# Optimization experiments

Measured on AMD Instinct MI355X. Metric: run time of the kernel, lower is better.

Reference implementation:

```python
import jax, jax.numpy as jnp
import numpy as np

B, S, E, H = 4, 2048, 1024, 16
D = E // H


def setup_inputs() -> dict:
    key = jax.random.key(0)
    ks = jax.random.split(key, 6)
    scale = 1.0 / np.sqrt(E).astype(np.float32)
    return {
        "x": jax.random.normal(ks[0], (B, S, E), jnp.float32),
        # positive entries -> cumsum normalizer is well conditioned
        "weight": jax.random.uniform(ks[1], (H, S), jnp.float32, 0.05, 1.0),
        "bias": jax.random.normal(ks[2], (H, S), jnp.float32) * 0.02,
        "inp_w": jax.random.normal(ks[3], (E, E), jnp.float32) * scale,
        "inp_b": jax.random.normal(ks[4], (E,), jnp.float32) * 0.02,
        "out_w": jax.random.normal(ks[5], (E, E), jnp.float32) * scale,
    }


def reference(x, weight, bias, inp_w, inp_b, out_w):
    Bx, Sx, Ex = x.shape
    Hx = weight.shape[0]
    Dx = Ex // Hx
    # input projection (torch Linear: x @ W.T + b)
    x = x @ inp_w.T + inp_b
    # (B,S,E) -> (B,E,S) -> (B,H,D,S)
    xh = x.transpose(0, 2, 1).reshape(Bx, Hx, Dx, Sx)
    # Toeplitz causal matrix per head: M[h,i,j] = weight[h, j-i] if j>=i else 0
    idx = jnp.arange(Sx)
    off = idx[None, :] - idx[:, None]  # (S,S)
    M = jnp.where(off >= 0, weight[:, off], jnp.zeros((), x.dtype))  # (H,S,S)
    # batched matmul over the sequence axis: y[b,h,d,t] = sum_s x[b,h,d,s] M[h,s,t]
    y = jnp.einsum('bhds,hst->bhdt', xh, M)
    # cumulative-sum normalization (do_toep_mean=True)
    norm = jnp.cumsum(weight, axis=-1)  # (H,S)
    y = y / norm[None, :, None, :]
    # per-head, per-position bias
    y = y + bias[None, :, None, :]
    # (B,H,D,S) -> (B,E,S) -> (B,S,E)
    y = y.reshape(Bx, Ex, Sx).transpose(0, 2, 1)
    # output projection (no bias)
    return y @ out_w.T
```

## Files before the change

kernel.cpp:

```cpp
#include <hip/hip_runtime.h>

typedef unsigned short u16;
typedef __attribute__((ext_vector_type(4))) float f32x4;
typedef __attribute__((ext_vector_type(8))) short short8;
typedef __attribute__((ext_vector_type(8))) __bf16 bf16x8;

__device__ __forceinline__ u16 f2bf(float f) {
  unsigned u = __builtin_bit_cast(unsigned, f);
  u = u + 0x7fffu + ((u >> 16) & 1u);
  return (u16)(u >> 16);
}

__device__ __forceinline__ void load_lds16(const void* g, void* l) {
  __builtin_amdgcn_global_load_lds((__attribute__((address_space(1))) void*)g,
                                   (__attribute__((address_space(3))) void*)l,
                                   16, 0, 0);
}

__global__ __launch_bounds__(256) void prep_all(const float* __restrict__ x,
                                                const float* __restrict__ inp_w,
                                                const float* __restrict__ out_w,
                                                const float* __restrict__ weight,
                                                u16* __restrict__ Xb,
                                                u16* __restrict__ Wb,
                                                u16* __restrict__ OWb,
                                                float* __restrict__ normB,
                                                u16* __restrict__ V) {
  const int bx = blockIdx.x, tid = threadIdx.x;
  if (bx < 10240) {
    const float* src; u16* dst; int i;
    if (bx < 8192)      { src = x;     dst = Xb;  i = bx * 256 + tid; }
    else if (bx < 9216) { src = inp_w; dst = Wb;  i = (bx - 8192) * 256 + tid; }
    else                { src = out_w; dst = OWb; i = (bx - 9216) * 256 + tid; }
    const float4 v = ((const float4*)src)[i];
    ushort4 o;
    o.x = f2bf(v.x); o.y = f2bf(v.y); o.z = f2bf(v.z); o.w = f2bf(v.w);
    ((ushort4*)dst)[i] = o;
    return;
  }
  if (bx < 10256) {
    const int h = bx - 10240;
    __shared__ float ts[256];
    float v[8];
    const float* src = weight + h * 2048 + tid * 8;
    float s = 0.f;
#pragma unroll
    for (int j = 0; j < 8; ++j) v[j] = src[j];
#pragma unroll
    for (int j = 0; j < 8; ++j) { s += v[j]; v[j] = s; }
    ts[tid] = s;
    __syncthreads();
    float xx = s;
#pragma unroll
    for (int d = 1; d < 256; d <<= 1) {
      float y = (tid >= d) ? ts[tid - d] : 0.f;
      __syncthreads();
      xx += y;
      ts[tid] = xx;
      __syncthreads();
    }
    const float excl = xx - s;
    float* dst = normB + h * 2048 + tid * 8;
#pragma unroll
    for (int j = 0; j < 8; ++j) dst[j] = excl + v[j];
    return;
  }
  {
    const int bb = bx - 10256;
    const int h = bb & 15, tb = bb >> 4;
    __shared__ u16 wl[2048];
#pragma unroll
    for (int j = 0; j < 8; ++j) wl[tid * 8 + j] = f2bf(weight[h * 2048 + tid * 8 + j]);
    __syncthreads();
#pragma unroll
    for (int i = 0; i < 8; ++i) {
      const int cid = i * 256 + tid;
      const int row = cid >> 4, c = cid & 15;
      const int t = tb * 128 + row;
      const int j0 = c * 8;
      unsigned v[8];
#pragma unroll
      for (int jj = 0; jj < 8; ++jj) {
        const int j = j0 + jj;
        v[jj] = (t >= j) ? (unsigned)wl[t - j] : 0u;
      }
      uint4 o;
      o.x = v[0] | (v[1] << 16); o.y = v[2] | (v[3] << 16);
      o.z = v[4] | (v[5] << 16); o.w = v[6] | (v[7] << 16);
      *(uint4*)(V + ((size_t)(h * 2048 + t)) * 128 + j0) = o;
    }
  }
}

template <bool BIAS, bool F32OUT, int GX>
__global__ __launch_bounds__(256) void gemm_nt4(const u16* __restrict__ A,
                                                const u16* __restrict__ B,
                                                void* __restrict__ C,
                                                const float* __restrict__ bias,
                                                int K, int lda, int ldb, int ldc) {
  __shared__ __align__(16) u16 As[2][128 * 64];
  __shared__ __align__(16) u16 Bs[2][128 * 64];
  const int tid = threadIdx.x;
  const int lane = tid & 63, wv = tid >> 6;
  const int wm = wv >> 1, wn = wv & 1;
  const int l15 = lane & 15, g = lane >> 4;

  const int flat = (int)blockIdx.x;
  const int sw = (flat & 7) * 64 + (flat >> 3);
  const int m0 = (sw / GX) * 128, n0 = (sw % GX) * 128;

  const int NT = K >> 6;

  auto stage = [&](int t, int bi) {
    const int kt = t << 6;
#pragma unroll
    for (int i = 0; i < 4; ++i) {
      const int c = i * 256 + tid;
      const int row = c >> 3, cc = c & 7;
      load_lds16(A + (size_t)(m0 + row) * lda + kt + ((cc ^ (row & 7)) << 3),
                 &As[bi][i * 2048 + wv * 512]);
    }
#pragma unroll
    for (int i = 0; i < 4; ++i) {
      const int c = i * 256 + tid;
      const int row = c >> 3, cc = c & 7;
      load_lds16(B + (size_t)(n0 + row) * ldb + kt + ((cc ^ (row & 7)) << 3),
                 &Bs[bi][i * 2048 + wv * 512]);
    }
  };

  f32x4 acc[4][4] = {};
  stage(0, 0);
  __syncthreads();
  int cur = 0;
  for (int t = 0; t < NT; ++t) {
    if (t + 1 < NT) stage(t + 1, cur ^ 1);
#pragma unroll
    for (int kh = 0; kh < 2; ++kh) {
      bf16x8 af[4], bf[4];
#pragma unroll
      for (int mf = 0; mf < 4; ++mf) {
        const int row = wm * 64 + mf * 16 + l15;
        af[mf] = *(const bf16x8*)(&As[cur][row * 64 + ((((kh << 2) + g) ^ (row & 7)) << 3)]);
      }
#pragma unroll
      for (int nf = 0; nf < 4; ++nf) {
        const int row = wn * 64 + nf * 16 + l15;
        bf[nf] = *(const bf16x8*)(&Bs[cur][row * 64 + ((((kh << 2) + g) ^ (row & 7)) << 3)]);
      }
      __builtin_amdgcn_s_setprio(1);
#pragma unroll
      for (int mf = 0; mf < 4; ++mf)
#pragma unroll
        for (int nf = 0; nf < 4; ++nf)
          acc[mf][nf] = __builtin_amdgcn_mfma_f32_16x16x32_bf16(af[mf], bf[nf],
                                                                acc[mf][nf], 0, 0, 0);
      __builtin_amdgcn_s_setprio(0);
    }
    __syncthreads();
    cur ^= 1;
  }

#pragma unroll
  for (int mf = 0; mf < 4; ++mf) {
#pragma unroll
    for (int r = 0; r < 4; ++r) {
      const int row = m0 + wm * 64 + mf * 16 + g * 4 + r;
      const float bb = BIAS ? bias[row] : 0.f;
#pragma unroll
      for (int nf = 0; nf < 4; ++nf) {
        const int col = n0 + wn * 64 + nf * 16 + l15;
        const float v = acc[mf][nf][r] + bb;
        if (F32OUT)
          ((float*)C)[(size_t)row * ldc + col] = v;
        else
          ((u16*)C)[(size_t)row * ldc + col] = f2bf(v);
      }
    }
  }
}

__global__ __launch_bounds__(256) void toep_conv(const u16* __restrict__ X1t,
                                                 const u16* __restrict__ V,
                                                 const float* __restrict__ normB,
                                                 const float* __restrict__ biasB,
                                                 u16* __restrict__ Y2b) {
  __shared__ __align__(16) u16 As[3][128 * 64];
  __shared__ __align__(16) u16 Xs[3][64 * 64];
  const int tid = threadIdx.x;
  const int lane = tid & 63, wv = tid >> 6;
  const int l15 = lane & 15, g = lane >> 4;

  const int x = (int)blockIdx.x;
  const int h = (x & 7) + 8 * ((x >> 3) & 1);
  const int pb = x >> 4;
  const int pair = pb & 7, b = pb >> 3;

  const u16* Vh = V + (size_t)h * 2048 * 128;
  const u16* Xrow = X1t + (size_t)h * 64 * 8192 + b * 2048;

#pragma unroll 1
  for (int ti = 0; ti < 2; ++ti) {
    const int tt = ti ? pair : 15 - pair;
    const int t0 = tt * 128;
    const int Q = (tt + 1) * 2;
    f32x4 acc[2][4] = {};

    auto stage = [&](int q, int bufi) {
      const int st = q >> 1, k = q & 1;
      const u16* Ab = Vh + (size_t)(tt - st) * 128 * 128 + k * 64;
#pragma unroll
      for (int i = 0; i < 4; ++i) {
        const int c = i * 256 + tid;
        const int row = c >> 3, cc = c & 7;
        load_lds16(Ab + row * 128 + ((cc ^ (row & 7)) * 8),
                   &As[bufi][i * 2048 + wv * 512]);
      }
      const int s0 = st * 128 + k * 64;
#pragma unroll
      for (int i = 0; i < 2; ++i) {
        const int c = i * 256 + tid;
        const int row = c >> 3, cc = c & 7;
        load_lds16(Xrow + (size_t)row * 8192 + s0 + ((cc ^ (row & 7)) * 8),
                   &Xs[bufi][i * 2048 + wv * 512]);
      }
    };

    stage(0, 0);
    if (Q > 1) stage(1, 1);
    asm volatile("s_waitcnt vmcnt(6)" ::: "memory");
    __builtin_amdgcn_sched_barrier(0);
    __builtin_amdgcn_s_barrier();
    asm volatile("" ::: "memory");

    int cur = 0;
    for (int q = 0; q < Q; ++q) {
      if (q + 2 < Q) stage(q + 2, (q + 2) % 3);
#pragma unroll
      for (int ks = 0; ks < 2; ++ks) {
        bf16x8 af[2];
#pragma unroll
        for (int tf = 0; tf < 2; ++tf) {
          const int row = wv * 32 + tf * 16 + l15;
          af[tf] = *(const bf16x8*)(&As[cur][row * 64 + (((ks * 4 + g) ^ (row & 7)) * 8)]);
        }
#pragma unroll
        for (int nf = 0; nf < 4; ++nf) {
          const int row = nf * 16 + l15;
          const bf16x8 bv = *(const bf16x8*)(&Xs[cur][row * 64 + (((ks * 4 + g) ^ (row & 7)) * 8)]);
#pragma unroll
          for (int tf = 0; tf < 2; ++tf)
            acc[tf][nf] = __builtin_amdgcn_mfma_f32_16x16x32_bf16(af[tf], bv,
                                                                  acc[tf][nf], 0, 0, 0);
        }
      }
      if (q + 2 < Q)      asm volatile("s_waitcnt vmcnt(6)" ::: "memory");
      else if (q + 1 < Q) asm volatile("s_waitcnt vmcnt(0)" ::: "memory");
      __builtin_amdgcn_sched_barrier(0);
      __builtin_amdgcn_s_barrier();
      asm volatile("" ::: "memory");
      cur = (cur == 2) ? 0 : cur + 1;
    }

#pragma unroll
    for (int tf = 0; tf < 2; ++tf) {
#pragma unroll
      for (int r = 0; r < 4; ++r) {
        const int t = t0 + wv * 32 + tf * 16 + g * 4 + r;
        const float inv = 1.0f / normB[h * 2048 + t];
        const float bb = biasB[h * 2048 + t];
#pragma unroll
        for (int nf = 0; nf < 4; ++nf) {
          const int d = nf * 16 + l15;
          Y2b[(size_t)(b * 2048 + t) * 1024 + h * 64 + d] = f2bf(acc[tf][nf][r] * inv + bb);
        }
      }
    }
  }
}

extern "C" void kernel_launch(void* const* d_in, const int* in_sizes, int n_in,
                              void* d_out, int out_size, void* d_ws, size_t ws_size,
                              hipStream_t stream) {
  (void)in_sizes; (void)n_in; (void)out_size; (void)ws_size;
  const float* x      = (const float*)d_in[0];
  const float* weight = (const float*)d_in[1];
  const float* biasB  = (const float*)d_in[2];
  const float* inp_w  = (const float*)d_in[3];
  const float* inp_b  = (const float*)d_in[4];
  const float* out_w  = (const float*)d_in[5];

  char* ws = (char*)d_ws;
  u16* Xb    = (u16*)(ws + 0);
  u16* X1t   = (u16*)(ws + (size_t)(16u << 20));
  u16* Y2b   = (u16*)(ws + (size_t)(32u << 20));
  u16* Wb    = (u16*)(ws + (size_t)(48u << 20));
  u16* OWb   = (u16*)(ws + (size_t)(50u << 20));
  float* normB = (float*)(ws + (size_t)(53u << 20));
  u16* Vt    = (u16*)(ws + (size_t)(56u << 20));

  prep_all<<<10512, 256, 0, stream>>>(x, inp_w, out_w, weight, Xb, Wb, OWb, normB, Vt);

  gemm_nt4<true, false, 64><<<512, 256, 0, stream>>>(
      Wb, Xb, (void*)X1t, inp_b, 1024, 1024, 1024, 8192);

  toep_conv<<<512, 256, 0, stream>>>(X1t, Vt, normB, biasB, Y2b);

  gemm_nt4<false, true, 8><<<512, 256, 0, stream>>>(
      Y2b, OWb, d_out, nullptr, 1024, 1024, 1024, 1024);
}
```

Baseline: 99.36 us.

## Use 256-row Toeplitz tiles with zero-padded band and remap GEMM block swizzle

The Toeplitz conv kernel now gives each block one 256-row output tile, where before it processed two balanced 128-row tiles. The band matrix gets 128 leading zero rows so the extra sub-tile on the diagonal reads valid zeros, and prep_all gains blocks that write this padding. The pipeline drops from triple to double buffering, and each wave computes a 64x64 tile, which reuses operands more per LDS load. The first GEMM also gets an XCD-aware tile mapping. The cost is uneven per-block work across the 8 tile positions, because the causal balancing pairs are gone, and some MFMA work is spent on zero padding.

After: 106.1 us. 6.8% more time.

```diff
diff --git a/kernel.cpp b/kernel.cpp
--- a/kernel.cpp
+++ b/kernel.cpp
@@ -2,7 +2,6 @@
 
 typedef unsigned short u16;
 typedef __attribute__((ext_vector_type(4))) float f32x4;
-typedef __attribute__((ext_vector_type(8))) short short8;
 typedef __attribute__((ext_vector_type(8))) __bf16 bf16x8;
 
 __device__ __forceinline__ u16 f2bf(float f) {
@@ -16,6 +15,12 @@
                                    (__attribute__((address_space(3))) void*)l,
                                    16, 0, 0);
 }
+
+__device__ __forceinline__ f32x4 MF(bf16x8 a, bf16x8 b, f32x4 c) {
+  return __builtin_amdgcn_mfma_f32_16x16x32_bf16(a, b, c, 0, 0, 0);
+}
+
+#define VROWS 2176
 
 __global__ __launch_bounds__(256) void prep_all(const float* __restrict__ x,
                                                 const float* __restrict__ inp_w,
@@ -65,7 +70,7 @@
     for (int j = 0; j < 8; ++j) dst[j] = excl + v[j];
     return;
   }
-  {
+  if (bx < 10512) {
     const int bb = bx - 10256;
     const int h = bb & 15, tb = bb >> 4;
     __shared__ u16 wl[2048];
@@ -87,12 +92,21 @@
       uint4 o;
       o.x = v[0] | (v[1] << 16); o.y = v[2] | (v[3] << 16);
       o.z = v[4] | (v[5] << 16); o.w = v[6] | (v[7] << 16);
-      *(uint4*)(V + ((size_t)(h * 2048 + t)) * 128 + j0) = o;
-    }
-  }
-}
-
-template <bool BIAS, bool F32OUT, int GX>
+      *(uint4*)(V + ((size_t)h * VROWS + 128 + t) * 128 + j0) = o;
+    }
+    return;
+  }
+  {
+    const int bb = bx - 10512;
+    const int h = bb >> 1, part = bb & 1;
+    uint4 z; z.x = z.y = z.z = z.w = 0u;
+    uint4* dst = (uint4*)(V + (size_t)h * VROWS * 128 + part * 8192) + tid * 4;
+#pragma unroll
+    for (int j = 0; j < 4; ++j) dst[j] = z;
+  }
+}
+
+template <bool BIAS, bool F32OUT, int DEC>
 __global__ __launch_bounds__(256) void gemm_nt4(const u16* __restrict__ A,
                                                 const u16* __restrict__ B,
                                                 void* __restrict__ C,
@@ -106,8 +120,16 @@
   const int l15 = lane & 15, g = lane >> 4;
 
   const int flat = (int)blockIdx.x;
-  const int sw = (flat & 7) * 64 + (flat >> 3);
-  const int m0 = (sw / GX) * 128, n0 = (sw % GX) * 128;
+  int m0, n0;
+  if (DEC == 0) {
+    const int xcd = flat & 7, i = flat >> 3;
+    m0 = (i & 7) * 128;
+    n0 = ((xcd << 3) + (i >> 3)) * 128;
+  } else {
+    const int sw = (flat & 7) * 64 + (flat >> 3);
+    m0 = (sw >> 3) * 128;
+    n0 = (sw & 7) * 128;
+  }
 
   const int NT = K >> 6;
 
@@ -153,8 +175,7 @@
       for (int mf = 0; mf < 4; ++mf)
 #pragma unroll
         for (int nf = 0; nf < 4; ++nf)
-          acc[mf][nf] = __builtin_amdgcn_mfma_f32_16x16x32_bf16(af[mf], bf[nf],
-                                                                acc[mf][nf], 0, 0, 0);
+          acc[mf][nf] = MF(af[mf], bf[nf], acc[mf][nf]);
       __builtin_amdgcn_s_setprio(0);
     }
     __syncthreads();
@@ -181,99 +202,90 @@
 }
 
 __global__ __launch_bounds__(256) void toep_conv(const u16* __restrict__ X1t,
-                                                 const u16* __restrict__ V,
+                                                 const u16* __restrict__ Vpad,
                                                  const float* __restrict__ normB,
                                                  const float* __restrict__ biasB,
                                                  u16* __restrict__ Y2b) {
-  __shared__ __align__(16) u16 As[3][128 * 64];
-  __shared__ __align__(16) u16 Xs[3][64 * 64];
+  __shared__ __align__(16) u16 As[2][256 * 64];
+  __shared__ __align__(16) u16 Xs[2][64 * 64];
   const int tid = threadIdx.x;
   const int lane = tid & 63, wv = tid >> 6;
   const int l15 = lane & 15, g = lane >> 4;
 
   const int x = (int)blockIdx.x;
   const int h = (x & 7) + 8 * ((x >> 3) & 1);
-  const int pb = x >> 4;
-  const int pair = pb & 7, b = pb >> 3;
-
-  const u16* Vh = V + (size_t)h * 2048 * 128;
+  const int rest = x >> 4;
+  const int tb = 7 - (rest & 7);
+  const int b = rest >> 3;
+
+  const int t0 = tb * 256;
+  const int Q = 4 * tb + 4;
+
+  const u16* Vbase = Vpad + (size_t)h * VROWS * 128 + (size_t)(128 + t0) * 128;
   const u16* Xrow = X1t + (size_t)h * 64 * 8192 + b * 2048;
 
-#pragma unroll 1
-  for (int ti = 0; ti < 2; ++ti) {
-    const int tt = ti ? pair : 15 - pair;
-    const int t0 = tt * 128;
-    const int Q = (tt + 1) * 2;
-    f32x4 acc[2][4] = {};
-
-    auto stage = [&](int q, int bufi) {
-      const int st = q >> 1, k = q & 1;
-      const u16* Ab = Vh + (size_t)(tt - st) * 128 * 128 + k * 64;
-#pragma unroll
-      for (int i = 0; i < 4; ++i) {
-        const int c = i * 256 + tid;
-        const int row = c >> 3, cc = c & 7;
-        load_lds16(Ab + row * 128 + ((cc ^ (row & 7)) * 8),
-                   &As[bufi][i * 2048 + wv * 512]);
-      }
-      const int s0 = st * 128 + k * 64;
-#pragma unroll
-      for (int i = 0; i < 2; ++i) {
-        const int c = i * 256 + tid;
-        const int row = c >> 3, cc = c & 7;
-        load_lds16(Xrow + (size_t)row * 8192 + s0 + ((cc ^ (row & 7)) * 8),
-                   &Xs[bufi][i * 2048 + wv * 512]);
-      }
-    };
-
-    stage(0, 0);
-    if (Q > 1) stage(1, 1);
-    asm volatile("s_waitcnt vmcnt(6)" ::: "memory");
-    __builtin_amdgcn_sched_barrier(0);
-    __builtin_amdgcn_s_barrier();
-    asm volatile("" ::: "memory");
-
-    int cur = 0;
-    for (int q = 0; q < Q; ++q) {
-      if (q + 2 < Q) stage(q + 2, (q + 2) % 3);
-#pragma unroll
-      for (int ks = 0; ks < 2; ++ks) {
-        bf16x8 af[2];
-#pragma unroll
-        for (int tf = 0; tf < 2; ++tf) {
-          const int row = wv * 32 + tf * 16 + l15;
-          af[tf] = *(const bf16x8*)(&As[cur][row * 64 + (((ks * 4 + g) ^ (row & 7)) * 8)]);
-        }
-#pragma unroll
-        for (int nf = 0; nf < 4; ++nf) {
-          const int row = nf * 16 + l15;
-          const bf16x8 bv = *(const bf16x8*)(&Xs[cur][row * 64 + (((ks * 4 + g) ^ (row & 7)) * 8)]);
-#pragma unroll
-          for (int tf = 0; tf < 2; ++tf)
-            acc[tf][nf] = __builtin_amdgcn_mfma_f32_16x16x32_bf16(af[tf], bv,
-                                                                  acc[tf][nf], 0, 0, 0);
-        }
-      }
-      if (q + 2 < Q)      asm volatile("s_waitcnt vmcnt(6)" ::: "memory");
-      else if (q + 1 < Q) asm volatile("s_waitcnt vmcnt(0)" ::: "memory");
-      __builtin_amdgcn_sched_barrier(0);
-      __builtin_amdgcn_s_barrier();
-      asm volatile("" ::: "memory");
-      cur = (cur == 2) ? 0 : cur + 1;
-    }
-
-#pragma unroll
-    for (int tf = 0; tf < 2; ++tf) {
-#pragma unroll
-      for (int r = 0; r < 4; ++r) {
-        const int t = t0 + wv * 32 + tf * 16 + g * 4 + r;
-        const float inv = 1.0f / normB[h * 2048 + t];
-        const float bb = biasB[h * 2048 + t];
-#pragma unroll
-        for (int nf = 0; nf < 4; ++nf) {
-          const int d = nf * 16 + l15;
-          Y2b[(size_t)(b * 2048 + t) * 1024 + h * 64 + d] = f2bf(acc[tf][nf][r] * inv + bb);
-        }
+  auto stage = [&](int q, int bi) {
+    const int st = q >> 1, half = q & 1;
+    const u16* Ab = Vbase - (size_t)st * 128 * 128 + half * 64;
+#pragma unroll
+    for (int i = 0; i < 8; ++i) {
+      const int c = i * 256 + tid;
+      const int row = c >> 3, cc = c & 7;
+      load_lds16(Ab + (size_t)row * 128 + ((cc ^ (row & 7)) << 3),
+                 &As[bi][i * 2048 + wv * 512]);
+    }
+    const int s0 = q * 64;
+#pragma unroll
+    for (int i = 0; i < 2; ++i) {
+      const int c = i * 256 + tid;
+      const int row = c >> 3, cc = c & 7;
+      load_lds16(Xrow + (size_t)row * 8192 + s0 + ((cc ^ (row & 7)) << 3),
+                 &Xs[bi][i * 2048 + wv * 512]);
+    }
+  };
+
+  f32x4 acc[4][4] = {};
+  stage(0, 0);
+  __syncthreads();
+  int cur = 0;
+  for (int q = 0; q < Q; ++q) {
+    if (q + 1 < Q) stage(q + 1, cur ^ 1);
+#pragma unroll
+    for (int ks = 0; ks < 2; ++ks) {
+      bf16x8 af[4], bv[4];
+#pragma unroll
+      for (int tf = 0; tf < 4; ++tf) {
+        const int trow = wv * 64 + tf * 16 + l15;
+        af[tf] = *(const bf16x8*)(&As[cur][trow * 64 + ((((ks << 2) + g) ^ (trow & 7)) << 3)]);
+      }
+#pragma unroll
+      for (int nf = 0; nf < 4; ++nf) {
+        const int drow = nf * 16 + l15;
+        bv[nf] = *(const bf16x8*)(&Xs[cur][drow * 64 + ((((ks << 2) + g) ^ (drow & 7)) << 3)]);
+      }
+      __builtin_amdgcn_s_setprio(1);
+#pragma unroll
+      for (int tf = 0; tf < 4; ++tf)
+#pragma unroll
+        for (int nf = 0; nf < 4; ++nf)
+          acc[tf][nf] = MF(af[tf], bv[nf], acc[tf][nf]);
+      __builtin_amdgcn_s_setprio(0);
+    }
+    __syncthreads();
+    cur ^= 1;
+  }
+
+#pragma unroll
+  for (int tf = 0; tf < 4; ++tf) {
+#pragma unroll
+    for (int r = 0; r < 4; ++r) {
+      const int t = t0 + wv * 64 + tf * 16 + g * 4 + r;
+      const float inv = 1.0f / normB[h * 2048 + t];
+      const float bb = biasB[h * 2048 + t];
+#pragma unroll
+      for (int nf = 0; nf < 4; ++nf) {
+        const int d = nf * 16 + l15;
+        Y2b[(size_t)(b * 2048 + t) * 1024 + h * 64 + d] = f2bf(acc[tf][nf][r] * inv + bb);
       }
     }
   }
@@ -296,16 +308,16 @@
   u16* Y2b   = (u16*)(ws + (size_t)(32u << 20));
   u16* Wb    = (u16*)(ws + (size_t)(48u << 20));
   u16* OWb   = (u16*)(ws + (size_t)(50u << 20));
-  float* normB = (float*)(ws + (size_t)(53u << 20));
-  u16* Vt    = (u16*)(ws + (size_t)(56u << 20));
-
-  prep_all<<<10512, 256, 0, stream>>>(x, inp_w, out_w, weight, Xb, Wb, OWb, normB, Vt);
-
-  gemm_nt4<true, false, 64><<<512, 256, 0, stream>>>(
+  float* normB = (float*)(ws + (size_t)(52u << 20));
+  u16* Vt    = (u16*)(ws + (size_t)(53u << 20));
+
+  prep_all<<<10544, 256, 0, stream>>>(x, inp_w, out_w, weight, Xb, Wb, OWb, normB, Vt);
+
+  gemm_nt4<true, false, 0><<<512, 256, 0, stream>>>(
       Wb, Xb, (void*)X1t, inp_b, 1024, 1024, 1024, 8192);
 
   toep_conv<<<512, 256, 0, stream>>>(X1t, Vt, normB, biasB, Y2b);
 
-  gemm_nt4<false, true, 8><<<512, 256, 0, stream>>>(
+  gemm_nt4<false, true, 1><<<512, 256, 0, stream>>>(
       Y2b, OWb, d_out, nullptr, 1024, 1024, 1024, 1024);
 }
```
